# Optimization experiments

Hardware: AMD Instinct MI355X
Metric: run time of the kernel (lower is better)

The kernel has to match this reference:

```python
import jax, jax.numpy as jnp
import numpy as np

B, C, N, K = 2, 128, 8192, 16
EPS = 1e-5
SLOPE = 0.2


def _knn_idx(coords, k):
    # coords: [B, 3, N] -> idx: [B, N, k] (k nearest neighbors, self excluded)
    pts = jnp.transpose(coords, (0, 2, 1))            # [B, N, 3]
    sq = jnp.sum(pts * pts, axis=-1)                  # [B, N]
    d2 = sq[:, :, None] + sq[:, None, :] - 2.0 * jnp.einsum('bnd,bmd->bnm', pts, pts)
    _, idx = jax.lax.top_k(-d2, k + 1)                # nearest first; first is self (dist 0)
    return idx[:, :, 1:]


def _graph_feature(feats, idx):
    # feats: [B, C, N], idx: [B, N, k] -> [B, 2C, N, k] = concat(center, neighbor - center)
    gather = jax.vmap(lambda f, i: f[:, i])           # [C,N],[N,k] -> [C,N,k]
    neigh = gather(feats, idx)                        # [B, C, N, k]
    center = jnp.broadcast_to(feats[..., None], neigh.shape)
    return jnp.concatenate([center, neigh - center], axis=1)


def _inorm(x):
    # InstanceNorm2d, affine=False: normalize per (b, c) over spatial dims
    m = jnp.mean(x, axis=(2, 3), keepdims=True)
    v = jnp.var(x, axis=(2, 3), keepdims=True)
    return (x - m) * jax.lax.rsqrt(v + EPS)


def _block(x, W):
    # 1x1 conv (no bias) + instance norm + leaky relu
    y = jnp.einsum('oc,bcnk->bonk', W, x)
    return jax.nn.leaky_relu(_inorm(y), SLOPE)


def setup_inputs() -> dict:
    key = jax.random.key(0)
    k0, k1, k2, k3, k4 = jax.random.split(key, 5)
    coords = jax.random.normal(k0, (B, 3, N), dtype=jnp.float32)
    features = jax.random.normal(k1, (B, C, N), dtype=jnp.float32)
    W1 = jax.random.normal(k2, (C, 2 * C), dtype=jnp.float32) * 0.05
    W2 = jax.random.normal(k3, (2 * C, 2 * C), dtype=jnp.float32) * 0.05
    W3 = jax.random.normal(k4, (C, 4 * C), dtype=jnp.float32) * 0.05
    return {"coords": coords, "features": features, "W1": W1, "W2": W2, "W3": W3}


def reference(coords, features, W1, W2, W3):
    idx = _knn_idx(coords, K)                  # same coords for both gathers -> compute once
    x0 = features                              # [B, C, N]
    x1 = _block(_graph_feature(x0, idx), W1).max(axis=-1)   # [B, C, N]
    x2 = _block(_graph_feature(x1, idx), W2).max(axis=-1)   # [B, 2C, N]
    x3 = jnp.concatenate([x0, x1, x2], axis=1)              # [B, 4C, N]
    y = jnp.einsum('oc,bcn->bon', W3, x3)[..., None]        # [B, C, N, 1]
    out = jax.nn.leaky_relu(_inorm(y), SLOPE)[..., 0]       # [B, C, N]
    return out
```

## Files before the change

### kernel.cpp

```cpp
#include <hip/hip_runtime.h>
#include <math.h>

#define NB 2
#define NPTS 8192
#define CH 128
#define KNN 16
#define K17 17
#define EPSI 1e-5f
#define SLOPE 0.2f
#define NCH 32
#define CHSZ 256
#define SCAP 16
#define BIGF 3.0e38f

#define OFF_IDX   0L
#define OFF_X0B   1048576L
#define OFF_YM1   9437184L
#define OFF_YM2   17825792L
#define OFF_UV    34603008L
#define OFF_Y4    68157440L
#define OFF_SURV  OFF_X0B
#define OFF_PA    OFF_Y4
#define OFF_CNT   76546048L
#define OFF_TAU   78643200L
#define OFF_WM1   78708736L
#define OFF_WM2   78839808L
#define OFF_STATS 79101952L
#define OFF_SCB1  79110144L
#define OFF_SCB2  79112192L
#define OFF_PTS4  79116288L


__global__ void zero_stats_k(float* __restrict__ stats) {
  int t = blockIdx.x * 256 + threadIdx.x;
  if (t < 2048) stats[t] = 0.f;
}

__global__ void transpose_x0_k(const float* __restrict__ feat, float* __restrict__ x0b) {
  __shared__ float tile[32][33];
  int b = blockIdx.z;
  int n0 = blockIdx.x * 32, c0 = blockIdx.y * 32;
  int tx = threadIdx.x;
  for (int ty = threadIdx.y; ty < 32; ty += 8)
    tile[ty][tx] = feat[((long)b * CH + c0 + ty) * NPTS + n0 + tx];
  __syncthreads();
  for (int ty = threadIdx.y; ty < 32; ty += 8)
    x0b[((long)b * NPTS + n0 + ty) * 128 + c0 + tx] = tile[tx][ty];
}

__global__ void prep_w_k(const float* __restrict__ W1, const float* __restrict__ W2,
                         float* __restrict__ Wm1, float* __restrict__ Wm2) {
  int t = blockIdx.x * 256 + threadIdx.x;
  if (t < 256 * 128) {
    int r = t >> 7, k = t & 127;
    Wm1[t] = (r < 128) ? (W1[r * 256 + k] - W1[r * 256 + 128 + k])
                       : W1[(r - 128) * 256 + 128 + k];
  }
  if (t < 512 * 128) {
    int r = t >> 7, k = t & 127;
    Wm2[t] = (r < 256) ? (W2[r * 256 + k] - W2[r * 256 + 128 + k])
                       : W2[(r - 256) * 256 + 128 + k];
  }
}

__global__ void finalize_scb_k(const float* __restrict__ stats, float2* __restrict__ scb,
                               int count, float cinv) {
  int t = blockIdx.x * 256 + threadIdx.x;
  if (t < count) {
    float mean = stats[t * 2] * cinv;
    float var = stats[t * 2 + 1] * cinv - mean * mean;
    float inv = rsqrtf(var + EPSI);
    scb[t] = make_float2(inv, -mean * inv);
  }
}

__global__ void knn_prep_k(const float* __restrict__ coords, float4* __restrict__ pts) {
  int b = blockIdx.y;
  int i = blockIdx.x * 256 + threadIdx.x;
  const float* cb = coords + (long)b * 3 * NPTS;
  float x = cb[i], y = cb[NPTS + i], z = cb[2 * NPTS + i];
  float sq = __fadd_rn(__fadd_rn(__fmul_rn(x, x), __fmul_rn(y, y)), __fmul_rn(z, z));
  pts[(long)b * NPTS + i] = make_float4(x, y, z, sq);
}

#define DIST(pi, pj, d2)                                                          \
  float dot = __fadd_rn(__fadd_rn(__fmul_rn((pi).x, (pj).x), __fmul_rn((pi).y, (pj).y)), \
                        __fmul_rn((pi).z, (pj).z));                               \
  float d2 = __fsub_rn(__fadd_rn((pi).w, (pj).w), __fmul_rn(2.0f, dot));

#define KNN_INSERT(d2v, jv)                                              \
  if ((d2v) < d[K17 - 1]) {                                              \
    _Pragma("unroll")                                                    \
    for (int s = K17 - 1; s > 0; --s) {                                  \
      if ((d2v) < d[s - 1]) { d[s] = d[s - 1]; id[s] = id[s - 1]; }      \
      else if ((d2v) < d[s]) { d[s] = (d2v); id[s] = (jv); }             \
    }                                                                    \
    if ((d2v) < d[0]) { d[0] = (d2v); id[0] = (jv); }                    \
  }

__global__ __launch_bounds__(256) void knn_phaseA_k(const float4* __restrict__ pts,
                                                    float2* __restrict__ pa) {
  int b = blockIdx.y;
  int ib = blockIdx.x & 127;
  int sg = blockIdx.x >> 7;
  int i = ib * 64 + (threadIdx.x & 63);
  int sub = sg * 4 + (threadIdx.x >> 6);
  const float4* P = pts + (long)b * NPTS;
  float4 pi = P[i];
  float d0 = BIGF, d1 = BIGF;
  int i0 = 0x7fffffff, i1 = 0x7fffffff;
  int j0 = sub * 64;
  for (int jj = 0; jj < 64; ++jj) {
    float4 pj = P[j0 + jj];
    DIST(pi, pj, d2)
    if (d2 < d1) {
      if (d2 < d0) { d1 = d0; i1 = i0; d0 = d2; i0 = j0 + jj; }
      else { d1 = d2; i1 = j0 + jj; }
    }
  }
  long base = (((long)b * NPTS + i) * 32 + sub) * 2;
  pa[base] = make_float2(d0, __int_as_float(i0));
  pa[base + 1] = make_float2(d1, __int_as_float(i1));
}

__global__ __launch_bounds__(256) void knn_mergeA_k(const float2* __restrict__ pa,
                                                    float* __restrict__ tau) {
  int b = blockIdx.y;
  int i = blockIdx.x * 256 + threadIdx.x;
  float d[K17]; int id[K17];
#pragma unroll
  for (int s = 0; s < K17; ++s) { d[s] = BIGF; id[s] = 0x7fffffff; }
  long base = ((long)b * NPTS + i) * 64;
  for (int c = 0; c < 64; ++c) {
    float2 v = pa[base + c];
    if (v.x < d[K17 - 1]) {
      int j = __float_as_int(v.y);
      KNN_INSERT(v.x, j);
    }
  }
  tau[(long)b * NPTS + i] = d[K17 - 1];
}

__global__ __launch_bounds__(256) void knn_filter_k(const float4* __restrict__ pts,
                                                    const float* __restrict__ tau,
                                                    float2* __restrict__ surv,
                                                    int* __restrict__ counts) {
  int b = blockIdx.z;
  int i = blockIdx.x * 256 + threadIdx.x;
  int chunk = blockIdx.y;
  const float4* P = pts + (long)b * NPTS;
  float4 pi = P[i];
  float t = tau[(long)b * NPTS + i];
  long sbase = (((long)b * NPTS + i) * NCH + chunk) * SCAP;
  int cnt = 0;
  int j0 = chunk * CHSZ;
#pragma unroll 2
  for (int jj = 0; jj < CHSZ; ++jj) {
    float4 pj = P[j0 + jj];
    DIST(pi, pj, d2)
    if (d2 <= t) {
      if (cnt < SCAP) surv[sbase + cnt] = make_float2(d2, __int_as_float(j0 + jj));
      cnt++;
    }
  }
  counts[((long)b * NPTS + i) * NCH + chunk] = cnt;
}

__global__ __launch_bounds__(256) void knn_mergeB_k(const float2* __restrict__ surv,
                                                    const int* __restrict__ counts,
                                                    const float4* __restrict__ pts,
                                                    int* __restrict__ idxo) {
  __shared__ float2 lds[8][K17][32];
  int b = blockIdx.y;
  int pl = threadIdx.x & 31;
  int sub = threadIdx.x >> 5;
  int i = blockIdx.x * 32 + pl;
  const float4* P = pts + (long)b * NPTS;
  float4 pi = P[i];
  float d[K17]; int id[K17];
#pragma unroll
  for (int s = 0; s < K17; ++s) { d[s] = BIGF; id[s] = 0x7fffffff; }
  long cbase = ((long)b * NPTS + i) * NCH;
  int4 c4 = *(const int4*)(counts + cbase + sub * 4);
  int cnt4[4] = {c4.x, c4.y, c4.z, c4.w};
#pragma unroll
  for (int q = 0; q < 4; ++q) {
    int c = sub * 4 + q;
    int cnt = cnt4[q];
    if (cnt > SCAP) {
      int j0 = c * CHSZ;
      for (int jj = 0; jj < CHSZ; ++jj) {
        float4 pj = P[j0 + jj];
        DIST(pi, pj, d2)
        KNN_INSERT(d2, j0 + jj);
      }
    } else {
      long sb = (cbase + c) * SCAP;
      for (int p = 0; p < cnt; p += 2) {
        float4 v2 = *(const float4*)(surv + sb + p);
        if (v2.x < d[K17 - 1]) {
          int j = __float_as_int(v2.y);
          KNN_INSERT(v2.x, j);
        }
        if (p + 1 < cnt && v2.z < d[K17 - 1]) {
          int j = __float_as_int(v2.w);
          KNN_INSERT(v2.z, j);
        }
      }
    }
  }
#pragma unroll
  for (int s = 0; s < K17; ++s) lds[sub][s][pl] = make_float2(d[s], __int_as_float(id[s]));
  __syncthreads();
  if ((sub & 1) == 0) {
#pragma unroll
    for (int s = 0; s < K17; ++s) {
      float2 v = lds[sub + 1][s][pl];
      if (v.x < d[K17 - 1]) {
        int j = __float_as_int(v.y);
        KNN_INSERT(v.x, j);
      }
    }
  }
  __syncthreads();
  if ((sub & 1) == 0) {
#pragma unroll
    for (int s = 0; s < K17; ++s) lds[sub >> 1][s][pl] = make_float2(d[s], __int_as_float(id[s]));
  }
  __syncthreads();
  if (sub < 2) {
#pragma unroll
    for (int s = 0; s < K17; ++s) {
      float2 v = lds[2 * sub][s][pl];
      d[s] = v.x; id[s] = __float_as_int(v.y);
    }
#pragma unroll
    for (int s = 0; s < K17; ++s) {
      float2 v = lds[2 * sub + 1][s][pl];
      if (v.x < d[K17 - 1]) {
        int j = __float_as_int(v.y);
        KNN_INSERT(v.x, j);
      }
    }
  }
  __syncthreads();
  if (sub < 2) {
#pragma unroll
    for (int s = 0; s < K17; ++s) lds[sub][s][pl] = make_float2(d[s], __int_as_float(id[s]));
  }
  __syncthreads();
  if (sub == 0) {
#pragma unroll
    for (int s = 0; s < K17; ++s) {
      float2 v = lds[0][s][pl];
      d[s] = v.x; id[s] = __float_as_int(v.y);
    }
#pragma unroll
    for (int s = 0; s < K17; ++s) {
      float2 v = lds[1][s][pl];
      if (v.x < d[K17 - 1]) {
        int j = __float_as_int(v.y);
        KNN_INSERT(v.x, j);
      }
    }
    long ob = ((long)b * NPTS + i) * KNN;
#pragma unroll
    for (int s = 1; s < K17; ++s) idxo[ob + s - 1] = id[s];
  }
}

#define GBN 128
#define GBM 64
#define GBK 32
__global__ __launch_bounds__(256) void gemm_xt_k(const float* __restrict__ X, int sx, long xbs,
                                                 const float* __restrict__ W, int K,
                                                 float* __restrict__ Out, int so, long obs) {
  __shared__ float Xs[GBK][GBN + 4];
  __shared__ float Ws[GBK][GBM + 4];
  int b = blockIdx.z;
  const float* Xb = X + (long)b * xbs;
  float* Ob = Out + (long)b * obs;
  int n0 = blockIdx.x * GBN, m0 = blockIdx.y * GBM;
  int tx = threadIdx.x, ty = threadIdx.y;
  int tid = ty * 16 + tx;
  float acc[8][4];
#pragma unroll
  for (int i = 0; i < 8; ++i)
#pragma unroll
    for (int j = 0; j < 4; ++j) acc[i][j] = 0.f;

  for (int k0 = 0; k0 < K; k0 += GBK) {
#pragma unroll
    for (int i = 0; i < 4; ++i) {
      int q = tid + i * 256;
      int r = q >> 3, kq = (q & 7) * 4;
      const float4 v = *(const float4*)(Xb + (long)(n0 + r) * sx + k0 + kq);
      Xs[kq][r] = v.x; Xs[kq + 1][r] = v.y; Xs[kq + 2][r] = v.z; Xs[kq + 3][r] = v.w;
    }
#pragma unroll
    for (int i = 0; i < 2; ++i) {
      int q = tid + i * 256;
      int r = q >> 3, kq = (q & 7) * 4;
      const float4 v = *(const float4*)(W + (long)(m0 + r) * K + k0 + kq);
      Ws[kq][r] = v.x; Ws[kq + 1][r] = v.y; Ws[kq + 2][r] = v.z; Ws[kq + 3][r] = v.w;
    }
    __syncthreads();
#pragma unroll
    for (int kk = 0; kk < GBK; ++kk) {
      float4 w4 = *(const float4*)&Ws[kk][tx * 4];
      float4 xa = *(const float4*)&Xs[kk][ty * 8];
      float4 xb4 = *(const float4*)&Xs[kk][ty * 8 + 4];
      float xs[8] = {xa.x, xa.y, xa.z, xa.w, xb4.x, xb4.y, xb4.z, xb4.w};
      float wv[4] = {w4.x, w4.y, w4.z, w4.w};
#pragma unroll
      for (int i = 0; i < 8; ++i)
#pragma unroll
        for (int j = 0; j < 4; ++j) acc[i][j] = fmaf(xs[i], wv[j], acc[i][j]);
    }
    __syncthreads();
  }
#pragma unroll
  for (int i = 0; i < 8; ++i) {
    float4 v = make_float4(acc[i][0], acc[i][1], acc[i][2], acc[i][3]);
    *(float4*)(Ob + (long)(n0 + ty * 8 + i) * so + m0 + tx * 4) = v;
  }
}

#define AFFLK4(v, a0, a1, a2, a3)                              \
  v.x = fmaf(v.x, a0.x, a0.y); v.x = fmaxf(v.x, SLOPE * v.x);  \
  v.y = fmaf(v.y, a1.x, a1.y); v.y = fmaxf(v.y, SLOPE * v.y);  \
  v.z = fmaf(v.z, a2.x, a2.y); v.z = fmaxf(v.z, SLOPE * v.z);  \
  v.w = fmaf(v.w, a3.x, a3.y); v.w = fmaxf(v.w, SLOPE * v.w);

__global__ __launch_bounds__(256) void gemm_aff_k(const float* __restrict__ X,
                                                  const float2* __restrict__ scb,
                                                  const float* __restrict__ W,
                                                  float* __restrict__ Out, int so, long obs) {
  __shared__ float Xs[GBK][GBN + 4];
  __shared__ float Ws[GBK][GBM + 4];
  int b = blockIdx.z;
  const float* Xb = X + (long)b * NPTS * 128;
  const float2* sc = scb + b * 128;
  float* Ob = Out + (long)b * obs;
  int n0 = blockIdx.x * GBN, m0 = blockIdx.y * GBM;
  int tx = threadIdx.x, ty = threadIdx.y;
  int tid = ty * 16 + tx;
  float acc[8][4];
#pragma unroll
  for (int i = 0; i < 8; ++i)
#pragma unroll
    for (int j = 0; j < 4; ++j) acc[i][j] = 0.f;

  for (int k0 = 0; k0 < 128; k0 += GBK) {
#pragma unroll
    for (int i = 0; i < 4; ++i) {
      int q = tid + i * 256;
      int r = q >> 3, kq = (q & 7) * 4;
      float4 v = *(const float4*)(Xb + (long)(n0 + r) * 128 + k0 + kq);
      float2 a0 = sc[k0 + kq], a1 = sc[k0 + kq + 1], a2 = sc[k0 + kq + 2], a3 = sc[k0 + kq + 3];
      AFFLK4(v, a0, a1, a2, a3)
      Xs[kq][r] = v.x; Xs[kq + 1][r] = v.y; Xs[kq + 2][r] = v.z; Xs[kq + 3][r] = v.w;
    }
#pragma unroll
    for (int i = 0; i < 2; ++i) {
      int q = tid + i * 256;
      int r = q >> 3, kq = (q & 7) * 4;
      const float4 v = *(const float4*)(W + (long)(m0 + r) * 128 + k0 + kq);
      Ws[kq][r] = v.x; Ws[kq + 1][r] = v.y; Ws[kq + 2][r] = v.z; Ws[kq + 3][r] = v.w;
    }
    __syncthreads();
#pragma unroll
    for (int kk = 0; kk < GBK; ++kk) {
      float4 w4 = *(const float4*)&Ws[kk][tx * 4];
      float4 xa = *(const float4*)&Xs[kk][ty * 8];
      float4 xb4 = *(const float4*)&Xs[kk][ty * 8 + 4];
      float xs[8] = {xa.x, xa.y, xa.z, xa.w, xb4.x, xb4.y, xb4.z, xb4.w};
      float wv[4] = {w4.x, w4.y, w4.z, w4.w};
#pragma unroll
      for (int i = 0; i < 8; ++i)
#pragma unroll
        for (int j = 0; j < 4; ++j) acc[i][j] = fmaf(xs[i], wv[j], acc[i][j]);
    }
    __syncthreads();
  }
#pragma unroll
  for (int i = 0; i < 8; ++i) {
    float4 v = make_float4(acc[i][0], acc[i][1], acc[i][2], acc[i][3]);
    *(float4*)(Ob + (long)(n0 + ty * 8 + i) * so + m0 + tx * 4) = v;
  }
}

__global__ __launch_bounds__(256) void gemm_cat_k(const float* __restrict__ x0b,
                                                  const float* __restrict__ ym1,
                                                  const float* __restrict__ ym2,
                                                  const float2* __restrict__ scb1,
                                                  const float2* __restrict__ scb2,
                                                  const float* __restrict__ W,
                                                  float* __restrict__ OutA,
                                                  float* __restrict__ OutB) {
  __shared__ float Xs[GBK][GBN + 4];
  __shared__ float Ws[GBK][GBM + 4];
  int b = blockIdx.z;
  int mt = blockIdx.y & 1;
  int kh = blockIdx.y >> 1;
  float* Ob = (kh ? OutB : OutA) + (long)b * NPTS * 128;
  int n0 = blockIdx.x * GBN, m0 = mt * GBM;
  int tx = threadIdx.x, ty = threadIdx.y;
  int tid = ty * 16 + tx;
  float acc[8][4];
#pragma unroll
  for (int i = 0; i < 8; ++i)
#pragma unroll
    for (int j = 0; j < 4; ++j) acc[i][j] = 0.f;

  for (int ks = 0; ks < 8; ++ks) {
    int k0 = kh * 256 + ks * GBK;
    const float* Xb; long st_; const float2* sc_; int cb_;
    if (k0 < 128)      { Xb = x0b + (long)b * NPTS * 128; st_ = 128; sc_ = nullptr;        cb_ = 0; }
    else if (k0 < 256) { Xb = ym1 + (long)b * NPTS * 128; st_ = 128; sc_ = scb1 + b * 128; cb_ = 128; }
    else               { Xb = ym2 + (long)b * NPTS * 256; st_ = 256; sc_ = scb2 + b * 256; cb_ = 256; }
    int kl = k0 - cb_;
#pragma unroll
    for (int i = 0; i < 4; ++i) {
      int q = tid + i * 256;
      int r = q >> 3, kq = (q & 7) * 4;
      float4 v = *(const float4*)(Xb + (long)(n0 + r) * st_ + kl + kq);
      if (sc_) {
        float2 a0 = sc_[kl + kq], a1 = sc_[kl + kq + 1], a2 = sc_[kl + kq + 2], a3 = sc_[kl + kq + 3];
        AFFLK4(v, a0, a1, a2, a3)
      }
      Xs[kq][r] = v.x; Xs[kq + 1][r] = v.y; Xs[kq + 2][r] = v.z; Xs[kq + 3][r] = v.w;
    }
#pragma unroll
    for (int i = 0; i < 2; ++i) {
      int q = tid + i * 256;
      int r = q >> 3, kq = (q & 7) * 4;
      const float4 v = *(const float4*)(W + (long)(m0 + r) * 512 + k0 + kq);
      Ws[kq][r] = v.x; Ws[kq + 1][r] = v.y; Ws[kq + 2][r] = v.z; Ws[kq + 3][r] = v.w;
    }
    __syncthreads();
#pragma unroll
    for (int kk = 0; kk < GBK; ++kk) {
      float4 w4 = *(const float4*)&Ws[kk][tx * 4];
      float4 xa = *(const float4*)&Xs[kk][ty * 8];
      float4 xb4 = *(const float4*)&Xs[kk][ty * 8 + 4];
      float xs[8] = {xa.x, xa.y, xa.z, xa.w, xb4.x, xb4.y, xb4.z, xb4.w};
      float wv[4] = {w4.x, w4.y, w4.z, w4.w};
#pragma unroll
      for (int i = 0; i < 8; ++i)
#pragma unroll
        for (int j = 0; j < 4; ++j) acc[i][j] = fmaf(xs[i], wv[j], acc[i][j]);
    }
    __syncthreads();
  }
#pragma unroll
  for (int i = 0; i < 8; ++i) {
    float4 v = make_float4(acc[i][0], acc[i][1], acc[i][2], acc[i][3]);
    *(float4*)(Ob + (long)(n0 + ty * 8 + i) * 128 + m0 + tx * 4) = v;
  }
}

template <int CTILE, int PPB>
__global__ __launch_bounds__(256) void edge_max_t(const float* __restrict__ uv, int S, int voff,
                                                  int Cout, const int* __restrict__ idx,
                                                  float* __restrict__ ymax,
                                                  float* __restrict__ stats) {
  constexpr int CG = CTILE / 4;
  constexpr int PSL = 256 / CG;
  __shared__ float ls[2][256][4];
  int blk = blockIdx.x;
  int c = (blk & 7) >> 1;
  int b = c >> 1;
  int ct = c & 1;
  int pblk = ((blk >> 3) << 1) | (blk & 1);
  int ch0 = ct * CTILE;
  const float* uvb = uv + (long)b * NPTS * S;
  const int* idxb = idx + (long)b * NPTS * KNN;
  float* ymb = ymax + (long)b * NPTS * Cout;
  int cg = threadIdx.x & (CG - 1);
  int ps = threadIdx.x / CG;
  int n0 = pblk * PPB;
  const float* vb = uvb + voff + ch0 + 4 * cg;
  float4 s = make_float4(0.f, 0.f, 0.f, 0.f);
  float4 s2 = make_float4(0.f, 0.f, 0.f, 0.f);
  for (int p = ps; p < PPB; p += PSL) {
    int n = n0 + p;
    const int* ip = idxb + n * KNN;
    int4 ia = *(const int4*)(ip);
    int4 ib4 = *(const int4*)(ip + 4);
    int4 ic = *(const int4*)(ip + 8);
    int4 id4 = *(const int4*)(ip + 12);
    int mi[KNN] = {ia.x, ia.y, ia.z, ia.w, ib4.x, ib4.y, ib4.z, ib4.w,
                   ic.x, ic.y, ic.z, ic.w, id4.x, id4.y, id4.z, id4.w};
    float4 u = *(const float4*)(uvb + (long)n * S + ch0 + 4 * cg);
    float4 mx = make_float4(-INFINITY, -INFINITY, -INFINITY, -INFINITY);
#pragma unroll
    for (int k = 0; k < KNN; ++k) {
      float4 v = *(const float4*)(vb + (long)mi[k] * S);
      float4 y;
      y.x = u.x + v.x; y.y = u.y + v.y; y.z = u.z + v.z; y.w = u.w + v.w;
      mx.x = fmaxf(mx.x, y.x); mx.y = fmaxf(mx.y, y.y);
      mx.z = fmaxf(mx.z, y.z); mx.w = fmaxf(mx.w, y.w);
      s.x += y.x; s.y += y.y; s.z += y.z; s.w += y.w;
      s2.x = fmaf(y.x, y.x, s2.x); s2.y = fmaf(y.y, y.y, s2.y);
      s2.z = fmaf(y.z, y.z, s2.z); s2.w = fmaf(y.w, y.w, s2.w);
    }
    *(float4*)(ymb + (long)n * Cout + ch0 + 4 * cg) = mx;
  }
  int t = threadIdx.x;
  ls[0][t][0] = s.x; ls[0][t][1] = s.y; ls[0][t][2] = s.z; ls[0][t][3] = s.w;
  ls[1][t][0] = s2.x; ls[1][t][1] = s2.y; ls[1][t][2] = s2.z; ls[1][t][3] = s2.w;
  __syncthreads();
  if (ps == 0) {
#pragma unroll
    for (int j = 1; j < PSL; ++j) {
      int q = j * CG + cg;
      s.x += ls[0][q][0]; s.y += ls[0][q][1]; s.z += ls[0][q][2]; s.w += ls[0][q][3];
      s2.x += ls[1][q][0]; s2.y += ls[1][q][1]; s2.z += ls[1][q][2]; s2.w += ls[1][q][3];
    }
    float* st = stats + ((long)b * Cout + ch0 + 4 * cg) * 2;
    atomicAdd(&st[0], s.x); atomicAdd(&st[1], s2.x);
    atomicAdd(&st[2], s.y); atomicAdd(&st[3], s2.y);
    atomicAdd(&st[4], s.z); atomicAdd(&st[5], s2.z);
    atomicAdd(&st[6], s.w); atomicAdd(&st[7], s2.w);
  }
}

__global__ void colstats2_k(float* __restrict__ y4, const float* __restrict__ y4b,
                            float* __restrict__ stats) {
  int b = blockIdx.y;
  int o = threadIdx.x & 127, slot = threadIdx.x >> 7;
  int n0 = blockIdx.x * 64;
  float s = 0.f, s2 = 0.f;
  for (int p = slot; p < 64; p += 2) {
    long off = ((long)b * NPTS + n0 + p) * 128 + o;
    float y = y4[off] + y4b[off];
    y4[off] = y;
    s += y;
    s2 = fmaf(y, y, s2);
  }
  float* st = stats + ((long)b * 128 + o) * 2;
  atomicAdd(&st[0], s);
  atomicAdd(&st[1], s2);
}

__global__ void final_k(const float* __restrict__ y3, const float* __restrict__ stats,
                        float* __restrict__ out) {
  __shared__ float tile[32][33];
  int b = blockIdx.z;
  int n0 = blockIdx.x * 32, o0 = blockIdx.y * 32;
  int tx = threadIdx.x;
  for (int ty = threadIdx.y; ty < 32; ty += 8) {
    int o = o0 + tx;
    const float* st = stats + ((long)b * 128 + o) * 2;
    float mean = st[0] * (1.f / 8192.f);
    float var = st[1] * (1.f / 8192.f) - mean * mean;
    float inv = rsqrtf(var + EPSI);
    float y = y3[((long)b * NPTS + n0 + ty) * 128 + o];
    float z = (y - mean) * inv;
    tile[ty][tx] = z >= 0.f ? z : SLOPE * z;
  }
  __syncthreads();
  for (int ty = threadIdx.y; ty < 32; ty += 8)
    out[((long)b * CH + o0 + ty) * NPTS + n0 + tx] = tile[tx][ty];
}

extern "C" void kernel_launch(void* const* d_in, const int* in_sizes, int n_in,
                              void* d_out, int out_size, void* d_ws, size_t ws_size,
                              hipStream_t stream) {
  const float* coords = (const float*)d_in[0];
  const float* features = (const float*)d_in[1];
  const float* W1 = (const float*)d_in[2];
  const float* W2 = (const float*)d_in[3];
  const float* W3 = (const float*)d_in[4];
  float* out = (float*)d_out;
  char* ws = (char*)d_ws;

  int* idx = (int*)(ws + OFF_IDX);
  float* x0b = (float*)(ws + OFF_X0B);
  float* ym1 = (float*)(ws + OFF_YM1);
  float* ym2 = (float*)(ws + OFF_YM2);
  float* uv = (float*)(ws + OFF_UV);
  float* y4 = (float*)(ws + OFF_Y4);
  float2* surv = (float2*)(ws + OFF_SURV);
  float2* pa = (float2*)(ws + OFF_PA);
  int* counts = (int*)(ws + OFF_CNT);
  float* tau = (float*)(ws + OFF_TAU);
  float* wm1 = (float*)(ws + OFF_WM1);
  float* wm2 = (float*)(ws + OFF_WM2);
  float* stats = (float*)(ws + OFF_STATS);
  float2* scb1 = (float2*)(ws + OFF_SCB1);
  float2* scb2 = (float2*)(ws + OFF_SCB2);
  float4* pts4 = (float4*)(ws + OFF_PTS4);

  zero_stats_k<<<8, 256, 0, stream>>>(stats);
  knn_prep_k<<<dim3(NPTS / 256, NB), 256, 0, stream>>>(coords, pts4);
  knn_phaseA_k<<<dim3(1024, NB), 256, 0, stream>>>(pts4, pa);
  knn_mergeA_k<<<dim3(NPTS / 256, NB), 256, 0, stream>>>(pa, tau);
  knn_filter_k<<<dim3(NPTS / 256, NCH, NB), 256, 0, stream>>>(pts4, tau, surv, counts);
  knn_mergeB_k<<<dim3(NPTS / 32, NB), 256, 0, stream>>>(surv, counts, pts4, idx);

  transpose_x0_k<<<dim3(NPTS / 32, CH / 32, NB), dim3(32, 8), 0, stream>>>(features, x0b);
  prep_w_k<<<256, 256, 0, stream>>>(W1, W2, wm1, wm2);

  gemm_xt_k<<<dim3(NPTS / GBN, 256 / GBM, NB), dim3(16, 16), 0, stream>>>(
      x0b, 128, (long)NPTS * 128, wm1, 128, uv, 256, (long)NPTS * 256);
  edge_max_t<64, 32><<<dim3(NPTS / 32 * 2 * NB), 256, 0, stream>>>(uv, 256, 128, 128, idx,
                                                                   ym1, stats);
  finalize_scb_k<<<1, 256, 0, stream>>>(stats, scb1, 256, 1.0f / 131072.0f);
  gemm_aff_k<<<dim3(NPTS / GBN, 512 / GBM, NB), dim3(16, 16), 0, stream>>>(
      ym1, scb1, wm2, uv, 512, (long)NPTS * 512);
  edge_max_t<128, 32><<<dim3(NPTS / 32 * 2 * NB), 256, 0, stream>>>(uv, 512, 256, 256, idx,
                                                                    ym2, stats + 512);
  finalize_scb_k<<<2, 256, 0, stream>>>(stats + 512, scb2, 512, 1.0f / 131072.0f);
  gemm_cat_k<<<dim3(NPTS / GBN, 4, NB), dim3(16, 16), 0, stream>>>(
      x0b, ym1, ym2, scb1, scb2, W3, y4, uv);
  colstats2_k<<<dim3(NPTS / 64, NB), 256, 0, stream>>>(y4, uv, stats + 1536);
  final_k<<<dim3(NPTS / 32, CH / 32, NB), dim3(32, 8), 0, stream>>>(y4, stats + 1536, out);
}
```

Baseline: 487.2 us.

## Merge independent KNN, transpose, weight-prep and first GEMM launches into fused kernels

Combines the KNN filter pass with the feature transpose and weight preprocessing into one launch, and runs the KNN final merge and the first GEMM as two block ranges of a single kernel. Because these stages have no data dependence on each other, they can share the GPU and fewer launches are needed. The survivor buffer moves to the uv region and its per-chunk capacity is halved, which cuts survivor memory traffic but sends more chunks to the brute-force rescan path. The GEMM output is redirected to the ym2 region so it does not overlap the survivor buffer.

```diff
diff --git a/kernel.cpp b/kernel.cpp
--- a/kernel.cpp
+++ b/kernel.cpp
@@ -10,7 +10,7 @@
 #define SLOPE 0.2f
 #define NCH 32
 #define CHSZ 256
-#define SCAP 16
+#define SCAP 8
 #define BIGF 3.0e38f
 
 #define OFF_IDX   0L
@@ -19,7 +19,7 @@
 #define OFF_YM2   17825792L
 #define OFF_UV    34603008L
 #define OFF_Y4    68157440L
-#define OFF_SURV  OFF_X0B
+#define OFF_SURV  OFF_UV
 #define OFF_PA    OFF_Y4
 #define OFF_CNT   76546048L
 #define OFF_TAU   78643200L
@@ -34,33 +34,6 @@
 __global__ void zero_stats_k(float* __restrict__ stats) {
   int t = blockIdx.x * 256 + threadIdx.x;
   if (t < 2048) stats[t] = 0.f;
-}
-
-__global__ void transpose_x0_k(const float* __restrict__ feat, float* __restrict__ x0b) {
-  __shared__ float tile[32][33];
-  int b = blockIdx.z;
-  int n0 = blockIdx.x * 32, c0 = blockIdx.y * 32;
-  int tx = threadIdx.x;
-  for (int ty = threadIdx.y; ty < 32; ty += 8)
-    tile[ty][tx] = feat[((long)b * CH + c0 + ty) * NPTS + n0 + tx];
-  __syncthreads();
-  for (int ty = threadIdx.y; ty < 32; ty += 8)
-    x0b[((long)b * NPTS + n0 + ty) * 128 + c0 + tx] = tile[tx][ty];
-}
-
-__global__ void prep_w_k(const float* __restrict__ W1, const float* __restrict__ W2,
-                         float* __restrict__ Wm1, float* __restrict__ Wm2) {
-  int t = blockIdx.x * 256 + threadIdx.x;
-  if (t < 256 * 128) {
-    int r = t >> 7, k = t & 127;
-    Wm1[t] = (r < 128) ? (W1[r * 256 + k] - W1[r * 256 + 128 + k])
-                       : W1[(r - 128) * 256 + 128 + k];
-  }
-  if (t < 512 * 128) {
-    int r = t >> 7, k = t & 127;
-    Wm2[t] = (r < 256) ? (W2[r * 256 + k] - W2[r * 256 + 128 + k])
-                       : W2[(r - 256) * 256 + 128 + k];
-  }
 }
 
 __global__ void finalize_scb_k(const float* __restrict__ stats, float2* __restrict__ scb,
@@ -141,188 +114,228 @@
   tau[(long)b * NPTS + i] = d[K17 - 1];
 }
 
-__global__ __launch_bounds__(256) void knn_filter_k(const float4* __restrict__ pts,
-                                                    const float* __restrict__ tau,
-                                                    float2* __restrict__ surv,
-                                                    int* __restrict__ counts) {
-  int b = blockIdx.z;
-  int i = blockIdx.x * 256 + threadIdx.x;
-  int chunk = blockIdx.y;
-  const float4* P = pts + (long)b * NPTS;
-  float4 pi = P[i];
-  float t = tau[(long)b * NPTS + i];
-  long sbase = (((long)b * NPTS + i) * NCH + chunk) * SCAP;
-  int cnt = 0;
-  int j0 = chunk * CHSZ;
+__global__ __launch_bounds__(256) void fuse1_k(const float4* __restrict__ pts,
+                                               const float* __restrict__ tau,
+                                               float2* __restrict__ surv,
+                                               int* __restrict__ counts,
+                                               const float* __restrict__ feat,
+                                               float* __restrict__ x0b,
+                                               const float* __restrict__ W1,
+                                               const float* __restrict__ W2,
+                                               float* __restrict__ Wm1,
+                                               float* __restrict__ Wm2) {
+  __shared__ float tile[32][33];
+  int blk = blockIdx.x;
+  int tid = threadIdx.x;
+  if (blk < 2048) {
+    int b = blk >> 10;
+    int chunk = (blk >> 5) & 31;
+    int i = (blk & 31) * 256 + tid;
+    const float4* P = pts + (long)b * NPTS;
+    float4 pi = P[i];
+    float t = tau[(long)b * NPTS + i];
+    long sbase = (((long)b * NPTS + i) * NCH + chunk) * SCAP;
+    int cnt = 0;
+    int j0 = chunk * CHSZ;
 #pragma unroll 2
-  for (int jj = 0; jj < CHSZ; ++jj) {
-    float4 pj = P[j0 + jj];
-    DIST(pi, pj, d2)
-    if (d2 <= t) {
-      if (cnt < SCAP) surv[sbase + cnt] = make_float2(d2, __int_as_float(j0 + jj));
-      cnt++;
-    }
-  }
-  counts[((long)b * NPTS + i) * NCH + chunk] = cnt;
-}
-
-__global__ __launch_bounds__(256) void knn_mergeB_k(const float2* __restrict__ surv,
-                                                    const int* __restrict__ counts,
-                                                    const float4* __restrict__ pts,
-                                                    int* __restrict__ idxo) {
-  __shared__ float2 lds[8][K17][32];
-  int b = blockIdx.y;
-  int pl = threadIdx.x & 31;
-  int sub = threadIdx.x >> 5;
-  int i = blockIdx.x * 32 + pl;
-  const float4* P = pts + (long)b * NPTS;
-  float4 pi = P[i];
-  float d[K17]; int id[K17];
-#pragma unroll
-  for (int s = 0; s < K17; ++s) { d[s] = BIGF; id[s] = 0x7fffffff; }
-  long cbase = ((long)b * NPTS + i) * NCH;
-  int4 c4 = *(const int4*)(counts + cbase + sub * 4);
-  int cnt4[4] = {c4.x, c4.y, c4.z, c4.w};
-#pragma unroll
-  for (int q = 0; q < 4; ++q) {
-    int c = sub * 4 + q;
-    int cnt = cnt4[q];
-    if (cnt > SCAP) {
-      int j0 = c * CHSZ;
-      for (int jj = 0; jj < CHSZ; ++jj) {
-        float4 pj = P[j0 + jj];
-        DIST(pi, pj, d2)
-        KNN_INSERT(d2, j0 + jj);
-      }
-    } else {
-      long sb = (cbase + c) * SCAP;
-      for (int p = 0; p < cnt; p += 2) {
-        float4 v2 = *(const float4*)(surv + sb + p);
-        if (v2.x < d[K17 - 1]) {
-          int j = __float_as_int(v2.y);
-          KNN_INSERT(v2.x, j);
-        }
-        if (p + 1 < cnt && v2.z < d[K17 - 1]) {
-          int j = __float_as_int(v2.w);
-          KNN_INSERT(v2.z, j);
-        }
-      }
-    }
-  }
-#pragma unroll
-  for (int s = 0; s < K17; ++s) lds[sub][s][pl] = make_float2(d[s], __int_as_float(id[s]));
-  __syncthreads();
-  if ((sub & 1) == 0) {
-#pragma unroll
-    for (int s = 0; s < K17; ++s) {
-      float2 v = lds[sub + 1][s][pl];
-      if (v.x < d[K17 - 1]) {
-        int j = __float_as_int(v.y);
-        KNN_INSERT(v.x, j);
-      }
-    }
-  }
-  __syncthreads();
-  if ((sub & 1) == 0) {
-#pragma unroll
-    for (int s = 0; s < K17; ++s) lds[sub >> 1][s][pl] = make_float2(d[s], __int_as_float(id[s]));
-  }
-  __syncthreads();
-  if (sub < 2) {
-#pragma unroll
-    for (int s = 0; s < K17; ++s) {
-      float2 v = lds[2 * sub][s][pl];
-      d[s] = v.x; id[s] = __float_as_int(v.y);
-    }
-#pragma unroll
-    for (int s = 0; s < K17; ++s) {
-      float2 v = lds[2 * sub + 1][s][pl];
-      if (v.x < d[K17 - 1]) {
-        int j = __float_as_int(v.y);
-        KNN_INSERT(v.x, j);
-      }
-    }
-  }
-  __syncthreads();
-  if (sub < 2) {
-#pragma unroll
-    for (int s = 0; s < K17; ++s) lds[sub][s][pl] = make_float2(d[s], __int_as_float(id[s]));
-  }
-  __syncthreads();
-  if (sub == 0) {
-#pragma unroll
-    for (int s = 0; s < K17; ++s) {
-      float2 v = lds[0][s][pl];
-      d[s] = v.x; id[s] = __float_as_int(v.y);
-    }
-#pragma unroll
-    for (int s = 0; s < K17; ++s) {
-      float2 v = lds[1][s][pl];
-      if (v.x < d[K17 - 1]) {
-        int j = __float_as_int(v.y);
-        KNN_INSERT(v.x, j);
-      }
-    }
-    long ob = ((long)b * NPTS + i) * KNN;
-#pragma unroll
-    for (int s = 1; s < K17; ++s) idxo[ob + s - 1] = id[s];
+    for (int jj = 0; jj < CHSZ; ++jj) {
+      float4 pj = P[j0 + jj];
+      DIST(pi, pj, d2)
+      if (d2 <= t) {
+        if (cnt < SCAP) surv[sbase + cnt] = make_float2(d2, __int_as_float(j0 + jj));
+        cnt++;
+      }
+    }
+    counts[((long)b * NPTS + i) * NCH + chunk] = cnt;
+  } else if (blk < 4096) {
+    int tb = blk - 2048;
+    int b = tb >> 10;
+    int n0 = (tb & 255) * 32;
+    int c0 = ((tb >> 8) & 3) * 32;
+    int tx = tid & 31, ty0 = tid >> 5;
+    for (int ty = ty0; ty < 32; ty += 8)
+      tile[ty][tx] = feat[((long)b * CH + c0 + ty) * NPTS + n0 + tx];
+    __syncthreads();
+    for (int ty = ty0; ty < 32; ty += 8)
+      x0b[((long)b * NPTS + n0 + ty) * 128 + c0 + tx] = tile[tx][ty];
+  } else {
+    int t = (blk - 4096) * 256 + tid;
+    if (t < 256 * 128) {
+      int r = t >> 7, k = t & 127;
+      Wm1[t] = (r < 128) ? (W1[r * 256 + k] - W1[r * 256 + 128 + k])
+                         : W1[(r - 128) * 256 + 128 + k];
+    }
+    if (t < 512 * 128) {
+      int r = t >> 7, k = t & 127;
+      Wm2[t] = (r < 256) ? (W2[r * 256 + k] - W2[r * 256 + 128 + k])
+                         : W2[(r - 256) * 256 + 128 + k];
+    }
   }
 }
 
 #define GBN 128
 #define GBM 64
 #define GBK 32
-__global__ __launch_bounds__(256) void gemm_xt_k(const float* __restrict__ X, int sx, long xbs,
-                                                 const float* __restrict__ W, int K,
-                                                 float* __restrict__ Out, int so, long obs) {
-  __shared__ float Xs[GBK][GBN + 4];
-  __shared__ float Ws[GBK][GBM + 4];
-  int b = blockIdx.z;
-  const float* Xb = X + (long)b * xbs;
-  float* Ob = Out + (long)b * obs;
-  int n0 = blockIdx.x * GBN, m0 = blockIdx.y * GBM;
-  int tx = threadIdx.x, ty = threadIdx.y;
-  int tid = ty * 16 + tx;
-  float acc[8][4];
-#pragma unroll
-  for (int i = 0; i < 8; ++i)
-#pragma unroll
-    for (int j = 0; j < 4; ++j) acc[i][j] = 0.f;
-
-  for (int k0 = 0; k0 < K; k0 += GBK) {
-#pragma unroll
-    for (int i = 0; i < 4; ++i) {
-      int q = tid + i * 256;
-      int r = q >> 3, kq = (q & 7) * 4;
-      const float4 v = *(const float4*)(Xb + (long)(n0 + r) * sx + k0 + kq);
-      Xs[kq][r] = v.x; Xs[kq + 1][r] = v.y; Xs[kq + 2][r] = v.z; Xs[kq + 3][r] = v.w;
-    }
-#pragma unroll
-    for (int i = 0; i < 2; ++i) {
-      int q = tid + i * 256;
-      int r = q >> 3, kq = (q & 7) * 4;
-      const float4 v = *(const float4*)(W + (long)(m0 + r) * K + k0 + kq);
-      Ws[kq][r] = v.x; Ws[kq + 1][r] = v.y; Ws[kq + 2][r] = v.z; Ws[kq + 3][r] = v.w;
-    }
-    __syncthreads();
-#pragma unroll
-    for (int kk = 0; kk < GBK; ++kk) {
-      float4 w4 = *(const float4*)&Ws[kk][tx * 4];
-      float4 xa = *(const float4*)&Xs[kk][ty * 8];
-      float4 xb4 = *(const float4*)&Xs[kk][ty * 8 + 4];
-      float xs[8] = {xa.x, xa.y, xa.z, xa.w, xb4.x, xb4.y, xb4.z, xb4.w};
-      float wv[4] = {w4.x, w4.y, w4.z, w4.w};
-#pragma unroll
-      for (int i = 0; i < 8; ++i)
-#pragma unroll
-        for (int j = 0; j < 4; ++j) acc[i][j] = fmaf(xs[i], wv[j], acc[i][j]);
-    }
-    __syncthreads();
-  }
-#pragma unroll
-  for (int i = 0; i < 8; ++i) {
-    float4 v = make_float4(acc[i][0], acc[i][1], acc[i][2], acc[i][3]);
-    *(float4*)(Ob + (long)(n0 + ty * 8 + i) * so + m0 + tx * 4) = v;
+__global__ __launch_bounds__(256) void fuse2_k(const float2* __restrict__ surv,
+                                               const int* __restrict__ counts,
+                                               const float4* __restrict__ pts,
+                                               int* __restrict__ idxo,
+                                               const float* __restrict__ x0b,
+                                               const float* __restrict__ wm1,
+                                               float* __restrict__ uv2) {
+  __shared__ char smem[8 * K17 * 32 * 8];
+  int blk = blockIdx.x;
+  int tid = threadIdx.x;
+  if (blk < 512) {
+    float2* Lm = (float2*)smem;
+#define LB(a, s, p) Lm[(((a) * K17) + (s)) * 32 + (p)]
+    int b = blk >> 8;
+    int pl = tid & 31;
+    int sub = tid >> 5;
+    int i = (blk & 255) * 32 + pl;
+    const float4* P = pts + (long)b * NPTS;
+    float4 pi = P[i];
+    float d[K17]; int id[K17];
+#pragma unroll
+    for (int s = 0; s < K17; ++s) { d[s] = BIGF; id[s] = 0x7fffffff; }
+    long cbase = ((long)b * NPTS + i) * NCH;
+    int4 c4 = *(const int4*)(counts + cbase + sub * 4);
+    int cnt4[4] = {c4.x, c4.y, c4.z, c4.w};
+#pragma unroll
+    for (int q = 0; q < 4; ++q) {
+      int c = sub * 4 + q;
+      int cnt = cnt4[q];
+      if (cnt > SCAP) {
+        int j0 = c * CHSZ;
+        for (int jj = 0; jj < CHSZ; ++jj) {
+          float4 pj = P[j0 + jj];
+          DIST(pi, pj, d2)
+          KNN_INSERT(d2, j0 + jj);
+        }
+      } else {
+        long sb = (cbase + c) * SCAP;
+        for (int p = 0; p < cnt; p += 2) {
+          float4 v2 = *(const float4*)(surv + sb + p);
+          if (v2.x < d[K17 - 1]) {
+            int j = __float_as_int(v2.y);
+            KNN_INSERT(v2.x, j);
+          }
+          if (p + 1 < cnt && v2.z < d[K17 - 1]) {
+            int j = __float_as_int(v2.w);
+            KNN_INSERT(v2.z, j);
+          }
+        }
+      }
+    }
+#pragma unroll
+    for (int s = 0; s < K17; ++s) LB(sub, s, pl) = make_float2(d[s], __int_as_float(id[s]));
+    __syncthreads();
+    if ((sub & 1) == 0) {
+#pragma unroll
+      for (int s = 0; s < K17; ++s) {
+        float2 v = LB(sub + 1, s, pl);
+        if (v.x < d[K17 - 1]) {
+          int j = __float_as_int(v.y);
+          KNN_INSERT(v.x, j);
+        }
+      }
+    }
+    __syncthreads();
+    if ((sub & 1) == 0) {
+#pragma unroll
+      for (int s = 0; s < K17; ++s) LB(sub >> 1, s, pl) = make_float2(d[s], __int_as_float(id[s]));
+    }
+    __syncthreads();
+    if (sub < 2) {
+#pragma unroll
+      for (int s = 0; s < K17; ++s) {
+        float2 v = LB(2 * sub, s, pl);
+        d[s] = v.x; id[s] = __float_as_int(v.y);
+      }
+#pragma unroll
+      for (int s = 0; s < K17; ++s) {
+        float2 v = LB(2 * sub + 1, s, pl);
+        if (v.x < d[K17 - 1]) {
+          int j = __float_as_int(v.y);
+          KNN_INSERT(v.x, j);
+        }
+      }
+    }
+    __syncthreads();
+    if (sub < 2) {
+#pragma unroll
+      for (int s = 0; s < K17; ++s) LB(sub, s, pl) = make_float2(d[s], __int_as_float(id[s]));
+    }
+    __syncthreads();
+    if (sub == 0) {
+#pragma unroll
+      for (int s = 0; s < K17; ++s) {
+        float2 v = LB(0, s, pl);
+        d[s] = v.x; id[s] = __float_as_int(v.y);
+      }
+#pragma unroll
+      for (int s = 0; s < K17; ++s) {
+        float2 v = LB(1, s, pl);
+        if (v.x < d[K17 - 1]) {
+          int j = __float_as_int(v.y);
+          KNN_INSERT(v.x, j);
+        }
+      }
+      long ob = ((long)b * NPTS + i) * KNN;
+#pragma unroll
+      for (int s = 1; s < K17; ++s) idxo[ob + s - 1] = id[s];
+    }
+#undef LB
+  } else {
+    float (*Xs)[GBN + 4] = (float (*)[GBN + 4])smem;
+    float (*Ws)[GBM + 4] = (float (*)[GBM + 4])(smem + sizeof(float) * GBK * (GBN + 4));
+    int g = blk - 512;
+    int b = g >> 8;
+    int n0 = (g & 63) * GBN, m0 = ((g >> 6) & 3) * GBM;
+    int tx = tid & 15, ty = tid >> 4;
+    const float* Xb = x0b + (long)b * NPTS * 128;
+    float* Ob = uv2 + (long)b * NPTS * 256;
+    float acc[8][4];
+#pragma unroll
+    for (int i = 0; i < 8; ++i)
+#pragma unroll
+      for (int j = 0; j < 4; ++j) acc[i][j] = 0.f;
+
+    for (int k0 = 0; k0 < 128; k0 += GBK) {
+#pragma unroll
+      for (int i = 0; i < 4; ++i) {
+        int q = tid + i * 256;
+        int r = q >> 3, kq = (q & 7) * 4;
+        const float4 v = *(const float4*)(Xb + (long)(n0 + r) * 128 + k0 + kq);
+        Xs[kq][r] = v.x; Xs[kq + 1][r] = v.y; Xs[kq + 2][r] = v.z; Xs[kq + 3][r] = v.w;
+      }
+#pragma unroll
+      for (int i = 0; i < 2; ++i) {
+        int q = tid + i * 256;
+        int r = q >> 3, kq = (q & 7) * 4;
+        const float4 v = *(const float4*)(wm1 + (long)(m0 + r) * 128 + k0 + kq);
+        Ws[kq][r] = v.x; Ws[kq + 1][r] = v.y; Ws[kq + 2][r] = v.z; Ws[kq + 3][r] = v.w;
+      }
+      __syncthreads();
+#pragma unroll
+      for (int kk = 0; kk < GBK; ++kk) {
+        float4 w4 = *(const float4*)&Ws[kk][tx * 4];
+        float4 xa = *(const float4*)&Xs[kk][ty * 8];
+        float4 xb4 = *(const float4*)&Xs[kk][ty * 8 + 4];
+        float xs[8] = {xa.x, xa.y, xa.z, xa.w, xb4.x, xb4.y, xb4.z, xb4.w};
+        float wv[4] = {w4.x, w4.y, w4.z, w4.w};
+#pragma unroll
+        for (int i = 0; i < 8; ++i)
+#pragma unroll
+          for (int j = 0; j < 4; ++j) acc[i][j] = fmaf(xs[i], wv[j], acc[i][j]);
+      }
+      __syncthreads();
+    }
+#pragma unroll
+    for (int i = 0; i < 8; ++i) {
+      float4 v = make_float4(acc[i][0], acc[i][1], acc[i][2], acc[i][3]);
+      *(float4*)(Ob + (long)(n0 + ty * 8 + i) * 256 + m0 + tx * 4) = v;
+    }
   }
 }
 
@@ -592,20 +605,16 @@
   float2* scb1 = (float2*)(ws + OFF_SCB1);
   float2* scb2 = (float2*)(ws + OFF_SCB2);
   float4* pts4 = (float4*)(ws + OFF_PTS4);
+  float* uv2 = ym2;
 
   zero_stats_k<<<8, 256, 0, stream>>>(stats);
   knn_prep_k<<<dim3(NPTS / 256, NB), 256, 0, stream>>>(coords, pts4);
   knn_phaseA_k<<<dim3(1024, NB), 256, 0, stream>>>(pts4, pa);
   knn_mergeA_k<<<dim3(NPTS / 256, NB), 256, 0, stream>>>(pa, tau);
-  knn_filter_k<<<dim3(NPTS / 256, NCH, NB), 256, 0, stream>>>(pts4, tau, surv, counts);
-  knn_mergeB_k<<<dim3(NPTS / 32, NB), 256, 0, stream>>>(surv, counts, pts4, idx);
-
-  transpose_x0_k<<<dim3(NPTS / 32, CH / 32, NB), dim3(32, 8), 0, stream>>>(features, x0b);
-  prep_w_k<<<256, 256, 0, stream>>>(W1, W2, wm1, wm2);
-
-  gemm_xt_k<<<dim3(NPTS / GBN, 256 / GBM, NB), dim3(16, 16), 0, stream>>>(
-      x0b, 128, (long)NPTS * 128, wm1, 128, uv, 256, (long)NPTS * 256);
-  edge_max_t<64, 32><<<dim3(NPTS / 32 * 2 * NB), 256, 0, stream>>>(uv, 256, 128, 128, idx,
+  fuse1_k<<<4352, 256, 0, stream>>>(pts4, tau, surv, counts, features, x0b, W1, W2, wm1,
+                                    wm2);
+  fuse2_k<<<1024, 256, 0, stream>>>(surv, counts, pts4, idx, x0b, wm1, uv2);
+  edge_max_t<64, 32><<<dim3(NPTS / 32 * 2 * NB), 256, 0, stream>>>(uv2, 256, 128, 128, idx,
                                                                    ym1, stats);
   finalize_scb_k<<<1, 256, 0, stream>>>(stats, scb1, 256, 1.0f / 131072.0f);
   gemm_aff_k<<<dim3(NPTS / GBN, 512 / GBM, NB), dim3(16, 16), 0, stream>>>(
```

Result: slower. 618.7 us (+27.0%).
